# Kernel tuning notes

Measured on AMD Instinct MI355X. Metric: run time of the kernel, lower is better.

## Reference

```python
import jax, jax.numpy as jnp
import numpy as np

H = 200  # hardcoded utterance_size == hidden_size in the module


def _lstm(Wih, Whh, bih, bhh, xs, h0, c0):
    """Run a torch-style LSTM (gate order i,f,g,o) over xs: [T,H] -> final hidden [H]."""
    b = bih + bhh
    def cell(carry, x):
        h, c = carry
        g = x @ Wih.T + h @ Whh.T + b
        i, f, gg, o = jnp.split(g, 4, axis=-1)
        c = jax.nn.sigmoid(f) * c + jax.nn.sigmoid(i) * jnp.tanh(gg)
        h = jax.nn.sigmoid(o) * jnp.tanh(c)
        return (h, c), None
    (h, _), _ = jax.lax.scan(cell, (h0, c0), xs)
    return h


def setup_inputs() -> dict:
    key = jax.random.key(0)
    S, W = 255, 512  # sentences (odd, so middle exists), words per sentence
    ks = jax.random.split(key, 24)
    d = {}
    d["utterances"] = jax.random.normal(ks[0], (S, W, H), jnp.float32)
    d["h0_sent"] = jax.random.normal(ks[1], (S, H), jnp.float32)  # per-sentence random h0 (torch.randn in original)
    d["h0_prev"] = jax.random.normal(ks[2], (H,), jnp.float32)
    d["h0_post"] = jax.random.normal(ks[3], (H,), jnp.float32)
    idx = 4
    for name in ["ctx", "main", "prev", "post"]:
        d[name + "_Wih"] = jax.random.normal(ks[idx], (4 * H, H), jnp.float32) * 0.05; idx += 1
        d[name + "_Whh"] = jax.random.normal(ks[idx], (4 * H, H), jnp.float32) * 0.05; idx += 1
        d[name + "_bih"] = jax.random.normal(ks[idx], (4 * H,), jnp.float32) * 0.05; idx += 1
        d[name + "_bhh"] = jax.random.normal(ks[idx], (4 * H,), jnp.float32) * 0.05; idx += 1
    d["fc_W"] = jax.random.normal(ks[idx], (H, 2 * H), jnp.float32) * 0.05
    d["fc_b"] = jnp.zeros((H,), jnp.float32)
    return d


def reference(utterances, h0_sent, h0_prev, h0_post,
              ctx_Wih, ctx_Whh, ctx_bih, ctx_bhh,
              main_Wih, main_Whh, main_bih, main_bhh,
              prev_Wih, prev_Whh, prev_bih, prev_bhh,
              post_Wih, post_Whh, post_bih, post_bhh,
              fc_W, fc_b):
    S = utterances.shape[0]
    mid = (S - 1) // 2
    z = jnp.zeros((H,), utterances.dtype)  # c0 = 0 for every LSTM
    # Context LSTM over every sentence (vectorized over sentences), word-level recurrence via scan.
    ctx_final = jax.vmap(
        lambda xs, h0: _lstm(ctx_Wih, ctx_Whh, ctx_bih, ctx_bhh, xs, h0, z)
    )(utterances, h0_sent)  # [S, H]
    # Middle sentence uses main_lstm instead.
    main_final = _lstm(main_Wih, main_Whh, main_bih, main_bhh,
                       utterances[mid], h0_sent[mid], z)  # [H]
    sent_emb = ctx_final.at[mid].set(main_final)  # [S, H]
    # prev_lstm runs over sentence embeddings 0..mid; prev_out = output at the middle step.
    prev_out = _lstm(prev_Wih, prev_Whh, prev_bih, prev_bhh,
                     sent_emb[:mid + 1], h0_prev, z)  # [H]
    # post_lstm runs reversed S-1..mid; post_out = output at the middle step.
    post_out = _lstm(post_Wih, post_Whh, post_bih, post_bhh,
                     sent_emb[mid:][::-1], h0_post, z)  # [H]
    feat = jnp.concatenate([prev_out, post_out])  # [2H]
    return feat @ fc_W.T + fc_b  # [H]
```

## Files before the change

kernel.cpp:

```cpp
#include <hip/hip_runtime.h>
#include <hip/hip_fp16.h>
#include <cstdint>

typedef _Float16 f16;
typedef _Float16 f16x2 __attribute__((ext_vector_type(2)));
typedef _Float16 f16x4 __attribute__((ext_vector_type(4)));
typedef _Float16 f16x8 __attribute__((ext_vector_type(8)));
typedef float f32x4 __attribute__((ext_vector_type(4)));

#define kH 200
#define kG 800
#define kS 255
#define kW 512
#define kMid 127

#define OFF_WF   209715200ULL
#define OFF_BS   212275200ULL
#define OFF_SENT 212288000ULL
#define OFF_XPP  212492032ULL
#define OFF_OUTS 212901632ULL

__device__ __forceinline__ float sigf(float x) { return 1.0f / (1.0f + __expf(-x)); }
__device__ __forceinline__ float tanhf_(float x) { return 1.0f - 2.0f / (__expf(2.0f * x) + 1.0f); }

__global__ __launch_bounds__(256) void ABHUE_prep(
    const float* W0, const float* W1, const float* W2, const float* W3,
    const float* W4, const float* W5, const float* W6, const float* W7,
    const float* B0i, const float* B0h, const float* B1i, const float* B1h,
    const float* B2i, const float* B2h, const float* B3i, const float* B3h,
    f16* wdst, float* bdst)
{
  int idx = blockIdx.x * 256 + threadIdx.x;
  const int WN = kG * kH;
  if (idx < 8 * WN) {
    int m = idx / WN, off = idx % WN;
    const float* src = m == 0 ? W0 : m == 1 ? W1 : m == 2 ? W2 : m == 3 ? W3
                     : m == 4 ? W4 : m == 5 ? W5 : m == 6 ? W6 : W7;
    wdst[idx] = (f16)src[off];
  } else {
    int j = idx - 8 * WN;
    if (j < 4 * kG) {
      int st = j / kG, k = j % kG;
      const float* bi = st == 0 ? B0i : st == 1 ? B1i : st == 2 ? B2i : B3i;
      const float* bh = st == 0 ? B0h : st == 1 ? B1h : st == 2 ? B2h : B3h;
      bdst[j] = bi[k] + bh[k];
    }
  }
}

#define BM 64
#define BKP 232
__global__ __launch_bounds__(256) void ABHUE_gemm_x(
    const float* __restrict__ A, const f16* __restrict__ Wf,
    const float* __restrict__ bias, f16* __restrict__ X, int rev)
{
  __shared__ __align__(16) f16 Al[BM * BKP];
  __shared__ __align__(16) f16 Bl[BM * BKP];
  int tid = threadIdx.x;
  int m0 = blockIdx.x * BM;

  #pragma unroll
  for (int it = 0; it < 4; ++it) {
    int idx = tid + 256 * it;
    int row = idx >> 4, dw = idx & 15;
    *(uint32_t*)(&Al[row * BKP + 200 + dw * 2]) = 0u;
    *(uint32_t*)(&Bl[row * BKP + 200 + dw * 2]) = 0u;
  }
  for (int it = 0; it < 13; ++it) {
    int q = tid + 256 * it;
    if (q < 3200) {
      int row = q / 50, c = q % 50;
      int rg = m0 + row; if (rev >= 0) rg = rev - rg;
      const float4 v = *(const float4*)(A + (size_t)rg * kH + c * 4);
      f16x2 p0; p0[0] = (f16)v.x; p0[1] = (f16)v.y;
      f16x2 p1; p1[0] = (f16)v.z; p1[1] = (f16)v.w;
      uint2 pk; pk.x = __builtin_bit_cast(uint32_t, p0); pk.y = __builtin_bit_cast(uint32_t, p1);
      *(uint2*)(&Al[row * BKP + c * 4]) = pk;
    }
  }
  int wv = tid >> 6, lane = tid & 63;
  int lr = lane & 15, lq = lane >> 4;

  for (int nt = 0; nt < 13; ++nt) {
    int n0 = nt * 64;
    __syncthreads();
    for (int it = 0; it < 7; ++it) {
      int q = tid + 256 * it;
      if (q < 1600) {
        int row = q / 25, c = q % 25;
        int ng = n0 + row;
        uint4 v = (ng < kG) ? *(const uint4*)(Wf + (size_t)ng * kH + c * 8)
                            : make_uint4(0, 0, 0, 0);
        *(uint4*)(&Bl[row * BKP + c * 8]) = v;
      }
    }
    __syncthreads();
    f32x4 acc0 = {0,0,0,0}, acc1 = {0,0,0,0}, acc2 = {0,0,0,0}, acc3 = {0,0,0,0};
    #pragma unroll
    for (int ks = 0; ks < 7; ++ks) {
      int k0 = ks * 32 + lq * 8;
      f16x8 a  = *(const f16x8*)(&Al[(wv * 16 + lr) * BKP + k0]);
      f16x8 b0 = *(const f16x8*)(&Bl[( 0 + lr) * BKP + k0]);
      f16x8 b1 = *(const f16x8*)(&Bl[(16 + lr) * BKP + k0]);
      f16x8 b2 = *(const f16x8*)(&Bl[(32 + lr) * BKP + k0]);
      f16x8 b3 = *(const f16x8*)(&Bl[(48 + lr) * BKP + k0]);
      acc0 = __builtin_amdgcn_mfma_f32_16x16x32_f16(a, b0, acc0, 0, 0, 0);
      acc1 = __builtin_amdgcn_mfma_f32_16x16x32_f16(a, b1, acc1, 0, 0, 0);
      acc2 = __builtin_amdgcn_mfma_f32_16x16x32_f16(a, b2, acc2, 0, 0, 0);
      acc3 = __builtin_amdgcn_mfma_f32_16x16x32_f16(a, b3, acc3, 0, 0, 0);
    }
    auto epi = [&](f32x4 acc, int nn) {
      int col = n0 + nn * 16 + lr;
      if (col < kG) {
        float bv = bias[col];
        #pragma unroll
        for (int rr = 0; rr < 4; ++rr) {
          int m = m0 + wv * 16 + lq * 4 + rr;
          X[(size_t)m * kG + col] = (f16)(acc[rr] + bv);
        }
      }
    };
    epi(acc0, 0); epi(acc1, 1); epi(acc2, 2); epi(acc3, 3);
  }
}

static __device__ void lstm_mfma(const f16* __restrict__ X, const f16* __restrict__ Whh,
                                 const float* __restrict__ h0, int nsteps,
                                 float* __restrict__ out)
{
  __shared__ __align__(16) f16 h_lds[224];
  __shared__ __align__(16) float gsh[kG];
  int tid = threadIdx.x;
  int lane = tid & 63, wv = tid >> 6;
  int lr = lane & 15, lq = lane >> 4;
  int t0 = (50 * wv) >> 3;
  int cnt = ((50 * (wv + 1)) >> 3) - t0;

  f16x8 bf[7][7];
  #pragma unroll
  for (int i = 0; i < 7; ++i) {
    if (i < cnt) {
      int n = (t0 + i) * 16 + lr;
      const f16* wrow = Whh + (size_t)n * kH;
      #pragma unroll
      for (int kt = 0; kt < 6; ++kt)
        bf[i][kt] = *(const f16x8*)(wrow + kt * 32 + lq * 8);
      bf[i][6] = (lq == 0) ? *(const f16x8*)(wrow + 192)
                           : (f16x8){0,0,0,0,0,0,0,0};
    }
  }

  f16x8 af[7];
  #pragma unroll
  for (int kt = 0; kt < 7; ++kt) af[kt] = (f16x8){0,0,0,0,0,0,0,0};

  if (tid < kH) h_lds[tid] = (f16)h0[tid];
  if (tid >= kH && tid < 224) h_lds[tid] = (f16)0;

  float cst = 0.f, hout = 0.f;
  f16 xc0 = (f16)0, xc1 = (f16)0, xc2 = (f16)0, xc3 = (f16)0;
  if (tid < kH) {
    xc0 = X[tid]; xc1 = X[kH + tid]; xc2 = X[2 * kH + tid]; xc3 = X[3 * kH + tid];
  }
  __syncthreads();

  for (int t = 0; t < nsteps; ++t) {
    f16 xn0 = (f16)0, xn1 = (f16)0, xn2 = (f16)0, xn3 = (f16)0;
    if (tid < kH && t + 1 < nsteps) {
      const f16* Xn = X + (size_t)(t + 1) * kG;
      xn0 = Xn[tid]; xn1 = Xn[kH + tid]; xn2 = Xn[2 * kH + tid]; xn3 = Xn[3 * kH + tid];
    }
    if (lr == 0) {
      #pragma unroll
      for (int kt = 0; kt < 7; ++kt)
        af[kt] = *(const f16x8*)(h_lds + kt * 32 + lq * 8);
    }
    #pragma unroll
    for (int i = 0; i < 7; ++i) {
      if (i < cnt) {
        f32x4 acc = {0.f, 0.f, 0.f, 0.f};
        #pragma unroll
        for (int kt = 0; kt < 7; ++kt)
          acc = __builtin_amdgcn_mfma_f32_16x16x32_f16(af[kt], bf[i][kt], acc, 0, 0, 0);
        if (lane < 16) {
          int n = (t0 + i) * 16 + lane;
          int g = n / kH, u = n - g * kH;
          gsh[u * 4 + g] = acc[0];
        }
      }
    }
    __syncthreads();
    if (tid < kH) {
      float4 gv = *(const float4*)(gsh + tid * 4);
      float gi = gv.x + (float)xc0;
      float gf = gv.y + (float)xc1;
      float gg = gv.z + (float)xc2;
      float go = gv.w + (float)xc3;
      cst  = sigf(gf) * cst + sigf(gi) * tanhf_(gg);
      hout = sigf(go) * tanhf_(cst);
      h_lds[tid] = (f16)hout;
    }
    xc0 = xn0; xc1 = xn1; xc2 = xn2; xc3 = xn3;
    __syncthreads();
  }
  if (out != nullptr && tid < kH) out[tid] = hout;
}

__global__ __launch_bounds__(512, 2) void ABHUE_lstm_batch(
    const f16* __restrict__ Xall, const f16* __restrict__ Wctx, const f16* __restrict__ Wmain,
    const float* __restrict__ h0s, float* __restrict__ sent)
{
  int s = blockIdx.x;
  const f16* X = Xall + (size_t)s * kW * kG;
  const f16* Wh = (s == 255) ? Wmain : Wctx;
  int hrow = (s == 255) ? kMid : s;
  const float* h0 = h0s + (size_t)hrow * kH;
  float* out = (s == kMid) ? nullptr : sent + (size_t)hrow * kH;
  lstm_mfma(X, Wh, h0, kW, out);
}

__global__ __launch_bounds__(512, 2) void ABHUE_lstm_pp(
    const f16* __restrict__ Xpp, const f16* __restrict__ Wprev, const f16* __restrict__ Wpost,
    const float* __restrict__ h0prev, const float* __restrict__ h0post, float* __restrict__ outs)
{
  int s = blockIdx.x;
  lstm_mfma(Xpp + (size_t)s * 128 * kG, s ? Wpost : Wprev, s ? h0post : h0prev, 128, outs + s * kH);
}

__global__ __launch_bounds__(256) void ABHUE_fc(
    const float* __restrict__ feat, const float* __restrict__ fcW,
    const float* __restrict__ fcb, float* __restrict__ outp)
{
  __shared__ float fs[2 * kH];
  int tid = threadIdx.x;
  for (int i = tid; i < 2 * kH; i += 256) fs[i] = feat[i];
  __syncthreads();
  if (tid < kH) {
    float acc = fcb[tid];
    #pragma unroll 4
    for (int j = 0; j < 2 * kH; ++j) acc = fmaf(fcW[tid * 2 * kH + j], fs[j], acc);
    outp[tid] = acc;
  }
}

extern "C" void kernel_launch(void* const* d_in, const int* in_sizes, int n_in,
                              void* d_out, int out_size, void* d_ws, size_t ws_size,
                              hipStream_t stream) {
  const float* utt    = (const float*)d_in[0];
  const float* h0s    = (const float*)d_in[1];
  const float* h0prev = (const float*)d_in[2];
  const float* h0post = (const float*)d_in[3];
  const float* wih[4] = {(const float*)d_in[4],  (const float*)d_in[8],
                         (const float*)d_in[12], (const float*)d_in[16]};
  const float* whh[4] = {(const float*)d_in[5],  (const float*)d_in[9],
                         (const float*)d_in[13], (const float*)d_in[17]};
  const float* bih[4] = {(const float*)d_in[6],  (const float*)d_in[10],
                         (const float*)d_in[14], (const float*)d_in[18]};
  const float* bhh[4] = {(const float*)d_in[7],  (const float*)d_in[11],
                         (const float*)d_in[15], (const float*)d_in[19]};
  const float* fcW = (const float*)d_in[20];
  const float* fcb = (const float*)d_in[21];

  char* base  = (char*)d_ws;
  f16*   Xall = (f16*)base;
  f16*   Wf   = (f16*)(base + OFF_WF);
  float* bsum = (float*)(base + OFF_BS);
  float* sent = (float*)(base + OFF_SENT);
  f16*   Xpp  = (f16*)(base + OFF_XPP);
  float* outs = (float*)(base + OFF_OUTS);

  const int WN = kG * kH;
  ABHUE_prep<<<(8 * WN + 4 * kG + 255) / 256, 256, 0, stream>>>(
      wih[0], whh[0], wih[1], whh[1], wih[2], whh[2], wih[3], whh[3],
      bih[0], bhh[0], bih[1], bhh[1], bih[2], bhh[2], bih[3], bhh[3],
      Wf, bsum);

  ABHUE_gemm_x<<<2040, 256, 0, stream>>>(utt, Wf + 0 * WN, bsum + 0, Xall, -1);
  ABHUE_gemm_x<<<8, 256, 0, stream>>>(utt + (size_t)kMid * kW * kH, Wf + 2 * WN,
                                      bsum + 800, Xall + (size_t)255 * kW * kG, -1);
  ABHUE_lstm_batch<<<256, 512, 0, stream>>>(Xall, Wf + 1 * WN, Wf + 3 * WN, h0s, sent);
  ABHUE_gemm_x<<<2, 256, 0, stream>>>(sent, Wf + 4 * WN, bsum + 1600, Xpp, -1);
  ABHUE_gemm_x<<<2, 256, 0, stream>>>(sent, Wf + 6 * WN, bsum + 2400, Xpp + (size_t)128 * kG, 254);
  ABHUE_lstm_pp<<<2, 512, 0, stream>>>(Xpp, Wf + 5 * WN, Wf + 7 * WN, h0prev, h0post, outs);
  ABHUE_fc<<<1, 256, 0, stream>>>(outs, fcW, fcb, (float*)d_out);
}
```

Baseline: 1.278 ms.

## Batch four sentences per LSTM block and interleave gate weights

The recurrent LSTM kernel now processes four sentences per workgroup, using four rows of the MFMA A operand instead of one. This cuts the block count from 256 to 65 and spreads the 50 gate tiles evenly as 7 per wave. Gate weights and biases are permuted in prep so the four gates of each hidden unit sit next to each other. Each thread then reads its x-projection with one 8-byte load, and the elementwise update covers 800 units using two per thread. The trade-off is much lower GPU occupancy (65 blocks on a 256-CU part), so per-step latency now dominates, and the sentence-to-row mapping logic becomes more complex.

Result: slower. 2.551 ms (+99.5%).

```diff
diff --git a/kernel.cpp b/kernel.cpp
--- a/kernel.cpp
+++ b/kernel.cpp
@@ -22,6 +22,18 @@
 
 __device__ __forceinline__ float sigf(float x) { return 1.0f / (1.0f + __expf(-x)); }
 __device__ __forceinline__ float tanhf_(float x) { return 1.0f - 2.0f / (__expf(2.0f * x) + 1.0f); }
+
+__device__ __forceinline__ const f16* sel4h(int s, const f16* a, const f16* b,
+                                            const f16* c, const f16* d) {
+  return s == 0 ? a : s == 1 ? b : s == 2 ? c : d;
+}
+__device__ __forceinline__ const float* sel4f(int s, const float* a, const float* b,
+                                              const float* c, const float* d) {
+  return s == 0 ? a : s == 1 ? b : s == 2 ? c : d;
+}
+__device__ __forceinline__ float* sel4o(int s, float* a, float* b, float* c, float* d) {
+  return s == 0 ? a : s == 1 ? b : s == 2 ? c : d;
+}
 
 __global__ __launch_bounds__(256) void ABHUE_prep(
     const float* W0, const float* W1, const float* W2, const float* W3,
@@ -36,14 +48,18 @@
     int m = idx / WN, off = idx % WN;
     const float* src = m == 0 ? W0 : m == 1 ? W1 : m == 2 ? W2 : m == 3 ? W3
                      : m == 4 ? W4 : m == 5 ? W5 : m == 6 ? W6 : W7;
-    wdst[idx] = (f16)src[off];
+    int np = off / kH, k = off - np * kH;
+    int u = np >> 2, g = np & 3;
+    wdst[idx] = (f16)src[(size_t)(g * kH + u) * kH + k];
   } else {
     int j = idx - 8 * WN;
     if (j < 4 * kG) {
-      int st = j / kG, k = j % kG;
+      int st = j / kG, np = j - st * kG;
+      int u = np >> 2, g = np & 3;
+      int n = g * kH + u;
       const float* bi = st == 0 ? B0i : st == 1 ? B1i : st == 2 ? B2i : B3i;
       const float* bh = st == 0 ? B0h : st == 1 ? B1h : st == 2 ? B2h : B3h;
-      bdst[j] = bi[k] + bh[k];
+      bdst[j] = bi[n] + bh[n];
     }
   }
 }
@@ -124,99 +140,144 @@
   }
 }
 
-static __device__ void lstm_mfma(const f16* __restrict__ X, const f16* __restrict__ Whh,
-                                 const float* __restrict__ h0, int nsteps,
-                                 float* __restrict__ out)
-{
-  __shared__ __align__(16) f16 h_lds[224];
-  __shared__ __align__(16) float gsh[kG];
+static __device__ void lstm_core4(const f16* x0, const f16* x1, const f16* x2, const f16* x3,
+                                  const f16* __restrict__ Whh,
+                                  const float* h00, const float* h01,
+                                  const float* h02, const float* h03,
+                                  float* o0, float* o1, float* o2, float* o3,
+                                  int nsteps)
+{
+  __shared__ __align__(16) f16 h_lds[4 * 232];
+  __shared__ __align__(16) float gsh[4 * kG];
   int tid = threadIdx.x;
   int lane = tid & 63, wv = tid >> 6;
   int lr = lane & 15, lq = lane >> 4;
-  int t0 = (50 * wv) >> 3;
-  int cnt = ((50 * (wv + 1)) >> 3) - t0;
 
   f16x8 bf[7][7];
   #pragma unroll
   for (int i = 0; i < 7; ++i) {
-    if (i < cnt) {
-      int n = (t0 + i) * 16 + lr;
-      const f16* wrow = Whh + (size_t)n * kH;
+    int tile = wv * 7 + i;
+    int n = tile * 16 + lr;
+    const f16* wrow = Whh + (size_t)n * kH;
+    bool real = (tile < 50);
+    #pragma unroll
+    for (int kt = 0; kt < 6; ++kt)
+      bf[i][kt] = real ? *(const f16x8*)(wrow + kt * 32 + lq * 8)
+                       : (f16x8){0,0,0,0,0,0,0,0};
+    bf[i][6] = (real && lq == 0) ? *(const f16x8*)(wrow + 192)
+                                 : (f16x8){0,0,0,0,0,0,0,0};
+  }
+
+  int q0 = tid, sp0 = q0 / kH, up0 = q0 - sp0 * kH;
+  bool v1 = (tid < 288);
+  int q1 = tid + 512; int sp1t = q1 / kH; int sp1 = sp1t > 3 ? 3 : sp1t;
+  int up1 = q1 - sp1t * kH; if (up1 < 0 || up1 >= kH) up1 = 0;
+  const f16* px0 = sel4h(sp0, x0, x1, x2, x3) + 4 * up0;
+  const f16* px1 = sel4h(sp1, x0, x1, x2, x3) + 4 * up1;
+  float* ow0 = sel4o(sp0, o0, o1, o2, o3);
+  float* ow1 = sel4o(sp1, o0, o1, o2, o3);
+  const float* ph0 = sel4f(sp0, h00, h01, h02, h03);
+  const float* ph1 = sel4f(sp1, h00, h01, h02, h03);
+
+  if (tid < 464) ((uint32_t*)h_lds)[tid] = 0u;
+  __syncthreads();
+  h_lds[sp0 * 232 + up0] = (f16)ph0[up0];
+  if (v1) h_lds[sp1 * 232 + up1] = (f16)ph1[up1];
+
+  float cA = 0.f, hA = 0.f, cB = 0.f, hB = 0.f;
+  uint2 xcA = *(const uint2*)px0;
+  uint2 xcB = v1 ? *(const uint2*)(px1) : make_uint2(0, 0);
+  __syncthreads();
+
+  for (int t = 0; t < nsteps; ++t) {
+    uint2 xnA = make_uint2(0, 0), xnB = make_uint2(0, 0);
+    if (t + 1 < nsteps) {
+      xnA = *(const uint2*)(px0 + (size_t)(t + 1) * kG);
+      if (v1) xnB = *(const uint2*)(px1 + (size_t)(t + 1) * kG);
+    }
+    f16x8 af[7];
+    #pragma unroll
+    for (int kt = 0; kt < 7; ++kt)
+      af[kt] = (lr < 4) ? *(const f16x8*)(h_lds + lr * 232 + kt * 32 + lq * 8)
+                        : (f16x8){0,0,0,0,0,0,0,0};
+    f32x4 acc[7];
+    #pragma unroll
+    for (int i = 0; i < 7; ++i) acc[i] = (f32x4){0.f, 0.f, 0.f, 0.f};
+    #pragma unroll
+    for (int kt = 0; kt < 7; ++kt) {
       #pragma unroll
-      for (int kt = 0; kt < 6; ++kt)
-        bf[i][kt] = *(const f16x8*)(wrow + kt * 32 + lq * 8);
-      bf[i][6] = (lq == 0) ? *(const f16x8*)(wrow + 192)
-                           : (f16x8){0,0,0,0,0,0,0,0};
-    }
-  }
-
-  f16x8 af[7];
-  #pragma unroll
-  for (int kt = 0; kt < 7; ++kt) af[kt] = (f16x8){0,0,0,0,0,0,0,0};
-
-  if (tid < kH) h_lds[tid] = (f16)h0[tid];
-  if (tid >= kH && tid < 224) h_lds[tid] = (f16)0;
-
-  float cst = 0.f, hout = 0.f;
-  f16 xc0 = (f16)0, xc1 = (f16)0, xc2 = (f16)0, xc3 = (f16)0;
-  if (tid < kH) {
-    xc0 = X[tid]; xc1 = X[kH + tid]; xc2 = X[2 * kH + tid]; xc3 = X[3 * kH + tid];
-  }
-  __syncthreads();
-
-  for (int t = 0; t < nsteps; ++t) {
-    f16 xn0 = (f16)0, xn1 = (f16)0, xn2 = (f16)0, xn3 = (f16)0;
-    if (tid < kH && t + 1 < nsteps) {
-      const f16* Xn = X + (size_t)(t + 1) * kG;
-      xn0 = Xn[tid]; xn1 = Xn[kH + tid]; xn2 = Xn[2 * kH + tid]; xn3 = Xn[3 * kH + tid];
-    }
-    if (lr == 0) {
+      for (int i = 0; i < 7; ++i)
+        acc[i] = __builtin_amdgcn_mfma_f32_16x16x32_f16(af[kt], bf[i][kt], acc[i], 0, 0, 0);
+    }
+    if (lq == 0) {
       #pragma unroll
-      for (int kt = 0; kt < 7; ++kt)
-        af[kt] = *(const f16x8*)(h_lds + kt * 32 + lq * 8);
-    }
-    #pragma unroll
-    for (int i = 0; i < 7; ++i) {
-      if (i < cnt) {
-        f32x4 acc = {0.f, 0.f, 0.f, 0.f};
-        #pragma unroll
-        for (int kt = 0; kt < 7; ++kt)
-          acc = __builtin_amdgcn_mfma_f32_16x16x32_f16(af[kt], bf[i][kt], acc, 0, 0, 0);
-        if (lane < 16) {
-          int n = (t0 + i) * 16 + lane;
-          int g = n / kH, u = n - g * kH;
-          gsh[u * 4 + g] = acc[0];
+      for (int i = 0; i < 7; ++i) {
+        int tile = wv * 7 + i;
+        if (tile < 50) {
+          int n = tile * 16 + lr;
+          gsh[0 * kG + n] = acc[i][0];
+          gsh[1 * kG + n] = acc[i][1];
+          gsh[2 * kG + n] = acc[i][2];
+          gsh[3 * kG + n] = acc[i][3];
         }
       }
     }
     __syncthreads();
-    if (tid < kH) {
-      float4 gv = *(const float4*)(gsh + tid * 4);
-      float gi = gv.x + (float)xc0;
-      float gf = gv.y + (float)xc1;
-      float gg = gv.z + (float)xc2;
-      float go = gv.w + (float)xc3;
-      cst  = sigf(gf) * cst + sigf(gi) * tanhf_(gg);
-      hout = sigf(go) * tanhf_(cst);
-      h_lds[tid] = (f16)hout;
-    }
-    xc0 = xn0; xc1 = xn1; xc2 = xn2; xc3 = xn3;
+    {
+      float4 gv = *(const float4*)(gsh + sp0 * kG + 4 * up0);
+      f16x4 xv = __builtin_bit_cast(f16x4, xcA);
+      float gi = gv.x + (float)xv[0];
+      float gf = gv.y + (float)xv[1];
+      float gg = gv.z + (float)xv[2];
+      float go = gv.w + (float)xv[3];
+      cA = sigf(gf) * cA + sigf(gi) * tanhf_(gg);
+      hA = sigf(go) * tanhf_(cA);
+      h_lds[sp0 * 232 + up0] = (f16)hA;
+    }
+    if (v1) {
+      float4 gv = *(const float4*)(gsh + sp1 * kG + 4 * up1);
+      f16x4 xv = __builtin_bit_cast(f16x4, xcB);
+      float gi = gv.x + (float)xv[0];
+      float gf = gv.y + (float)xv[1];
+      float gg = gv.z + (float)xv[2];
+      float go = gv.w + (float)xv[3];
+      cB = sigf(gf) * cB + sigf(gi) * tanhf_(gg);
+      hB = sigf(go) * tanhf_(cB);
+      h_lds[sp1 * 232 + up1] = (f16)hB;
+    }
+    xcA = xnA; xcB = xnB;
     __syncthreads();
   }
-  if (out != nullptr && tid < kH) out[tid] = hout;
+  if (ow0 != nullptr) ow0[up0] = hA;
+  if (v1 && ow1 != nullptr) ow1[up1] = hB;
 }
 
 __global__ __launch_bounds__(512, 2) void ABHUE_lstm_batch(
     const f16* __restrict__ Xall, const f16* __restrict__ Wctx, const f16* __restrict__ Wmain,
     const float* __restrict__ h0s, float* __restrict__ sent)
 {
-  int s = blockIdx.x;
-  const f16* X = Xall + (size_t)s * kW * kG;
-  const f16* Wh = (s == 255) ? Wmain : Wctx;
-  int hrow = (s == 255) ? kMid : s;
-  const float* h0 = h0s + (size_t)hrow * kH;
-  float* out = (s == kMid) ? nullptr : sent + (size_t)hrow * kH;
-  lstm_mfma(X, Wh, h0, kW, out);
+  int b = blockIdx.x;
+  if (b < 64) {
+    int s0 = 4 * b, s1 = s0 + 1, s2 = s0 + 2;
+    int s3 = (s0 + 3 > 254) ? 254 : s0 + 3;
+    const f16* x0 = Xall + (size_t)s0 * kW * kG;
+    const f16* x1 = Xall + (size_t)s1 * kW * kG;
+    const f16* x2 = Xall + (size_t)s2 * kW * kG;
+    const f16* x3 = Xall + (size_t)s3 * kW * kG;
+    float* o0 = (s0 == kMid) ? nullptr : sent + (size_t)s0 * kH;
+    float* o1 = (s1 == kMid) ? nullptr : sent + (size_t)s1 * kH;
+    float* o2 = (s2 == kMid) ? nullptr : sent + (size_t)s2 * kH;
+    float* o3 = (s3 == kMid || s0 + 3 > 254) ? nullptr : sent + (size_t)s3 * kH;
+    lstm_core4(x0, x1, x2, x3, Wctx,
+               h0s + (size_t)s0 * kH, h0s + (size_t)s1 * kH,
+               h0s + (size_t)s2 * kH, h0s + (size_t)s3 * kH,
+               o0, o1, o2, o3, kW);
+  } else {
+    const f16* xm = Xall + (size_t)255 * kW * kG;
+    const float* hm = h0s + (size_t)kMid * kH;
+    lstm_core4(xm, xm, xm, xm, Wmain, hm, hm, hm, hm,
+               sent + (size_t)kMid * kH, nullptr, nullptr, nullptr, kW);
+  }
 }
 
 __global__ __launch_bounds__(512, 2) void ABHUE_lstm_pp(
@@ -224,7 +285,10 @@
     const float* __restrict__ h0prev, const float* __restrict__ h0post, float* __restrict__ outs)
 {
   int s = blockIdx.x;
-  lstm_mfma(Xpp + (size_t)s * 128 * kG, s ? Wpost : Wprev, s ? h0post : h0prev, 128, outs + s * kH);
+  const f16* x = Xpp + (size_t)s * 128 * kG;
+  const float* h0 = s ? h0post : h0prev;
+  lstm_core4(x, x, x, x, s ? Wpost : Wprev, h0, h0, h0, h0,
+             outs + (size_t)s * kH, nullptr, nullptr, nullptr, 128);
 }
 
 __global__ __launch_bounds__(256) void ABHUE_fc(
@@ -278,7 +342,7 @@
   ABHUE_gemm_x<<<2040, 256, 0, stream>>>(utt, Wf + 0 * WN, bsum + 0, Xall, -1);
   ABHUE_gemm_x<<<8, 256, 0, stream>>>(utt + (size_t)kMid * kW * kH, Wf + 2 * WN,
                                       bsum + 800, Xall + (size_t)255 * kW * kG, -1);
-  ABHUE_lstm_batch<<<256, 512, 0, stream>>>(Xall, Wf + 1 * WN, Wf + 3 * WN, h0s, sent);
+  ABHUE_lstm_batch<<<65, 512, 0, stream>>>(Xall, Wf + 1 * WN, Wf + 3 * WN, h0s, sent);
   ABHUE_gemm_x<<<2, 256, 0, stream>>>(sent, Wf + 4 * WN, bsum + 1600, Xpp, -1);
   ABHUE_gemm_x<<<2, 256, 0, stream>>>(sent, Wf + 6 * WN, bsum + 2400, Xpp + (size_t)128 * kG, 254);
   ABHUE_lstm_pp<<<2, 512, 0, stream>>>(Xpp, Wf + 5 * WN, Wf + 7 * WN, h0prev, h0post, outs);
```

## Interleave gate weights so each wave owns its cells, removing a per-step barrier

Applied to the files above, without the earlier changes.

Weights and biases are permuted in the prep kernel into unit-major, gate-interleaved order, which also permutes the X projections. Each wave can then apply the LSTM cell update to exactly the gates it computed. The hidden state is double-buffered in LDS, and the mid-step __syncthreads is replaced by a wave-local lgkmcnt wait, so each time step needs one block barrier instead of two. The change also vectorizes the per-step X loads and issues the MFMA chains in independent pairs, at the cost of relying on the wave-to-cell partition staying wave-local.

Measured after the change: 1.309 ms. 2.4% more time.

```diff
diff --git a/kernel.cpp b/kernel.cpp
--- a/kernel.cpp
+++ b/kernel.cpp
@@ -36,14 +36,18 @@
     int m = idx / WN, off = idx % WN;
     const float* src = m == 0 ? W0 : m == 1 ? W1 : m == 2 ? W2 : m == 3 ? W3
                      : m == 4 ? W4 : m == 5 ? W5 : m == 6 ? W6 : W7;
-    wdst[idx] = (f16)src[off];
+    int np = off / kH, k = off - np * kH;
+    int u = np >> 2, g = np & 3;
+    wdst[idx] = (f16)src[(size_t)(g * kH + u) * kH + k];
   } else {
     int j = idx - 8 * WN;
     if (j < 4 * kG) {
-      int st = j / kG, k = j % kG;
+      int st = j / kG, np = j - st * kG;
+      int u = np >> 2, g = np & 3;
+      int n = g * kH + u;
       const float* bi = st == 0 ? B0i : st == 1 ? B1i : st == 2 ? B2i : B3i;
       const float* bh = st == 0 ? B0h : st == 1 ? B1h : st == 2 ? B2h : B3h;
-      bdst[j] = bi[k] + bh[k];
+      bdst[j] = bi[n] + bh[n];
     }
   }
 }
@@ -124,11 +128,11 @@
   }
 }
 
-static __device__ void lstm_mfma(const f16* __restrict__ X, const f16* __restrict__ Whh,
-                                 const float* __restrict__ h0, int nsteps,
-                                 float* __restrict__ out)
-{
-  __shared__ __align__(16) f16 h_lds[224];
+static __device__ void lstm_m1(const f16* __restrict__ X, const f16* __restrict__ Whh,
+                               const float* __restrict__ h0, int nsteps,
+                               float* __restrict__ out)
+{
+  __shared__ __align__(16) f16 hbuf[2][224];
   __shared__ __align__(16) float gsh[kG];
   int tid = threadIdx.x;
   int lane = tid & 63, wv = tid >> 6;
@@ -150,60 +154,65 @@
     }
   }
 
-  f16x8 af[7];
-  #pragma unroll
-  for (int kt = 0; kt < 7; ++kt) af[kt] = (f16x8){0,0,0,0,0,0,0,0};
-
-  if (tid < kH) h_lds[tid] = (f16)h0[tid];
-  if (tid >= kH && tid < 224) h_lds[tid] = (f16)0;
-
+  int ul = 4 * t0 + lane;
+  bool cellp = (lane < 4 * cnt);
+
+  if (tid < 24) { hbuf[0][200 + tid] = (f16)0; hbuf[1][200 + tid] = (f16)0; }
+  if (cellp) hbuf[0][ul] = (f16)h0[ul];
   float cst = 0.f, hout = 0.f;
-  f16 xc0 = (f16)0, xc1 = (f16)0, xc2 = (f16)0, xc3 = (f16)0;
-  if (tid < kH) {
-    xc0 = X[tid]; xc1 = X[kH + tid]; xc2 = X[2 * kH + tid]; xc3 = X[3 * kH + tid];
-  }
+  uint2 xc = make_uint2(0, 0);
+  if (cellp) xc = *(const uint2*)(X + 4 * ul);
   __syncthreads();
 
   for (int t = 0; t < nsteps; ++t) {
-    f16 xn0 = (f16)0, xn1 = (f16)0, xn2 = (f16)0, xn3 = (f16)0;
-    if (tid < kH && t + 1 < nsteps) {
-      const f16* Xn = X + (size_t)(t + 1) * kG;
-      xn0 = Xn[tid]; xn1 = Xn[kH + tid]; xn2 = Xn[2 * kH + tid]; xn3 = Xn[3 * kH + tid];
-    }
-    if (lr == 0) {
+    const f16* hb = hbuf[t & 1];
+    uint2 xn = make_uint2(0, 0);
+    if (cellp && t + 1 < nsteps)
+      xn = *(const uint2*)(X + (size_t)(t + 1) * kG + 4 * ul);
+
+    f16x8 af[7];
+    #pragma unroll
+    for (int kt = 0; kt < 7; ++kt)
+      af[kt] = *(const f16x8*)(hb + kt * 32 + lq * 8);
+
+    #pragma unroll
+    for (int ip = 0; ip < 3; ++ip) {
+      f32x4 a0 = {0.f,0.f,0.f,0.f}, a1 = {0.f,0.f,0.f,0.f};
+      #pragma unroll
+      for (int kt = 0; kt < 7; ++kt) {
+        a0 = __builtin_amdgcn_mfma_f32_16x16x32_f16(af[kt], bf[2*ip][kt], a0, 0, 0, 0);
+        a1 = __builtin_amdgcn_mfma_f32_16x16x32_f16(af[kt], bf[2*ip+1][kt], a1, 0, 0, 0);
+      }
+      if (lq == 0) {
+        gsh[(t0 + 2*ip) * 16 + lr]     = a0[0];
+        gsh[(t0 + 2*ip + 1) * 16 + lr] = a1[0];
+      }
+    }
+    if (cnt == 7) {
+      f32x4 a0 = {0.f,0.f,0.f,0.f};
       #pragma unroll
       for (int kt = 0; kt < 7; ++kt)
-        af[kt] = *(const f16x8*)(h_lds + kt * 32 + lq * 8);
-    }
-    #pragma unroll
-    for (int i = 0; i < 7; ++i) {
-      if (i < cnt) {
-        f32x4 acc = {0.f, 0.f, 0.f, 0.f};
-        #pragma unroll
-        for (int kt = 0; kt < 7; ++kt)
-          acc = __builtin_amdgcn_mfma_f32_16x16x32_f16(af[kt], bf[i][kt], acc, 0, 0, 0);
-        if (lane < 16) {
-          int n = (t0 + i) * 16 + lane;
-          int g = n / kH, u = n - g * kH;
-          gsh[u * 4 + g] = acc[0];
-        }
-      }
-    }
-    __syncthreads();
-    if (tid < kH) {
-      float4 gv = *(const float4*)(gsh + tid * 4);
-      float gi = gv.x + (float)xc0;
-      float gf = gv.y + (float)xc1;
-      float gg = gv.z + (float)xc2;
-      float go = gv.w + (float)xc3;
+        a0 = __builtin_amdgcn_mfma_f32_16x16x32_f16(af[kt], bf[6][kt], a0, 0, 0, 0);
+      if (lq == 0) gsh[(t0 + 6) * 16 + lr] = a0[0];
+    }
+
+    asm volatile("s_waitcnt lgkmcnt(0)" ::: "memory");
+
+    if (cellp) {
+      float4 gv = *(const float4*)(gsh + 4 * ul);
+      f16x4 xv = __builtin_bit_cast(f16x4, xc);
+      float gi = gv.x + (float)xv[0];
+      float gf = gv.y + (float)xv[1];
+      float gg = gv.z + (float)xv[2];
+      float go = gv.w + (float)xv[3];
       cst  = sigf(gf) * cst + sigf(gi) * tanhf_(gg);
       hout = sigf(go) * tanhf_(cst);
-      h_lds[tid] = (f16)hout;
-    }
-    xc0 = xn0; xc1 = xn1; xc2 = xn2; xc3 = xn3;
+      hbuf[(t & 1) ^ 1][ul] = (f16)hout;
+    }
+    xc = xn;
     __syncthreads();
   }
-  if (out != nullptr && tid < kH) out[tid] = hout;
+  if (out != nullptr && cellp) out[ul] = hout;
 }
 
 __global__ __launch_bounds__(512, 2) void ABHUE_lstm_batch(
@@ -216,7 +225,7 @@
   int hrow = (s == 255) ? kMid : s;
   const float* h0 = h0s + (size_t)hrow * kH;
   float* out = (s == kMid) ? nullptr : sent + (size_t)hrow * kH;
-  lstm_mfma(X, Wh, h0, kW, out);
+  lstm_m1(X, Wh, h0, kW, out);
 }
 
 __global__ __launch_bounds__(512, 2) void ABHUE_lstm_pp(
@@ -224,7 +233,8 @@
     const float* __restrict__ h0prev, const float* __restrict__ h0post, float* __restrict__ outs)
 {
   int s = blockIdx.x;
-  lstm_mfma(Xpp + (size_t)s * 128 * kG, s ? Wpost : Wprev, s ? h0post : h0prev, 128, outs + s * kH);
+  lstm_m1(Xpp + (size_t)s * 128 * kG, s ? Wpost : Wprev, s ? h0post : h0prev, 128,
+          outs + (size_t)s * kH);
 }
 
 __global__ __launch_bounds__(256) void ABHUE_fc(
```
